# Kernel optimization log

Measured on AMD Instinct MI355X. Metric: run time of the kernel, lower is better.

## Reference

```python
import jax, jax.numpy as jnp
import numpy as np

H, KV, D = 12, 4, 128  # n_head, n_kv_head, head_dim
VE_GATE_CH = 12

def _rmsnorm(x):
    eps = jnp.finfo(x.dtype).eps  # matches torch F.rms_norm default eps
    return x * jax.lax.rsqrt(jnp.mean(x * x, axis=-1, keepdims=True) + eps)

def _rope(x, cos, sin):
    d = x.shape[-1] // 2
    x1, x2 = x[..., :d], x[..., d:]
    return jnp.concatenate([x1 * cos + x2 * sin, -x1 * sin + x2 * cos], axis=-1)

def setup_inputs() -> dict:
    key = jax.random.key(0)
    ks = jax.random.split(key, 9)
    B, T, C = 2, 2048, 1536
    x = jax.random.normal(ks[0], (B, T, C), jnp.float32)
    ve = jax.random.normal(ks[1], (B, T, KV * D), jnp.float32)
    ang = jax.random.uniform(ks[2], (1, T, 1, D // 2), jnp.float32) * (2.0 * np.pi)
    cos, sin = jnp.cos(ang), jnp.sin(ang)
    Wq = jax.random.normal(ks[3], (H * D, C), jnp.float32) * 0.02
    Wk = jax.random.normal(ks[4], (KV * D, C), jnp.float32) * 0.02
    Wv = jax.random.normal(ks[5], (KV * D, C), jnp.float32) * 0.02
    Wproj = jax.random.normal(ks[6], (C, C), jnp.float32) * 0.02
    Wg = jax.random.normal(ks[7], (KV, VE_GATE_CH), jnp.float32) * 0.02
    return dict(x=x, ve=ve, cos=cos, sin=sin, Wq=Wq, Wk=Wk, Wv=Wv, Wproj=Wproj, Wg=Wg, window=1024)

def reference(x, ve, cos, sin, Wq, Wk, Wv, Wproj, Wg, window):
    B, T, C = x.shape
    q = (x @ Wq.T).reshape(B, T, H, D)
    k = (x @ Wk.T).reshape(B, T, KV, D)
    v = (x @ Wv.T).reshape(B, T, KV, D)
    # value-embedding gate: 3*sigmoid(Linear(x[..., :12])) per kv head
    gate = 3.0 * jax.nn.sigmoid(x[..., :VE_GATE_CH] @ Wg.T)  # [B,T,KV]
    v = v + gate[..., None] * ve.reshape(B, T, KV, D)
    q = _rmsnorm(_rope(q, cos, sin)) * 1.2
    k = _rmsnorm(_rope(k, cos, sin)) * 1.2
    rep = H // KV  # GQA group size
    qh = q.transpose(0, 2, 1, 3).reshape(B, KV, rep, T, D)
    kh = k.transpose(0, 2, 1, 3)  # [B,KV,T,D]
    vh = v.transpose(0, 2, 1, 3)
    scores = jnp.einsum('bgrtd,bgsd->bgrts', qh, kh) / np.sqrt(D)
    row = jnp.arange(T)[:, None]
    col = jnp.arange(T)[None, :]
    if window < 0 or window >= T:
        mask = col <= row  # pure causal
    else:
        mask = (col <= row) & (row - col <= window)  # causal sliding window
    scores = jnp.where(mask, scores, -jnp.inf)
    att = jax.nn.softmax(scores, axis=-1)
    y = jnp.einsum('bgrts,bgsd->bgrtd', att, vh)
    y = y.reshape(B, H, T, D).transpose(0, 2, 1, 3).reshape(B, T, H * D)
    return y @ Wproj.T
```

## Files before the change

kernel.cpp:

```cpp
#include <hip/hip_runtime.h>
#include <hip/hip_bf16.h>
#include <math.h>

#define B_  2
#define T_  2048
#define C_  1536
#define H_  12
#define KV_ 4
#define D_  128
#define M_  (B_*T_)
#define REP_ (H_/KV_)
#define NQKV_ 2560
#define KK_  1536
#define NKT_ 24

typedef __bf16 bf16x8 __attribute__((ext_vector_type(8)));
typedef float  f32x4  __attribute__((ext_vector_type(4)));
typedef unsigned u32x4 __attribute__((ext_vector_type(4)));

union BCast { u32x4 u; bf16x8 b; };

__device__ inline bf16x8 ldb8(const ushort* p) {
    BCast c; c.u = *reinterpret_cast<const u32x4*>(p); return c.b;
}

__device__ inline ushort f2bf(float f) {
    union { float f; unsigned u; } v; v.f = f;
    unsigned u = v.u;
    return (ushort)((u + 0x7FFF + ((u >> 16) & 1)) >> 16);
}

__device__ inline float bf2f(ushort u) {
    union { unsigned u; float f; } v; v.u = (unsigned)u << 16;
    return v.f;
}

__device__ inline void async_copy16(const ushort* g, ushort* l) {
    __builtin_amdgcn_global_load_lds(
        (const __attribute__((address_space(1))) unsigned*)g,
        (__attribute__((address_space(3))) unsigned*)l, 16, 0, 0);
}

__device__ __host__ inline int dperm(int d) {
    return (d < 32) ? d : (d < 64 ? d + 32 : (d < 96 ? d - 32 : d));
}

#define MFMA16(va, vb, d) d = __builtin_amdgcn_mfma_f32_16x16x32_bf16(va, vb, d, 0, 0, 0)

template<int EPI>
__global__ __launch_bounds__(256, 2) void gemm128(const ushort* __restrict__ A,
                                                  const ushort* __restrict__ Bm,
                                                  ushort* __restrict__ Qp,
                                                  ushort* __restrict__ Kp,
                                                  ushort* __restrict__ Vt,
                                                  float* __restrict__ Cf,
                                                  const float* __restrict__ cosb,
                                                  const float* __restrict__ sinb,
                                                  const float* __restrict__ xf,
                                                  const float* __restrict__ ve,
                                                  const float* __restrict__ Wg) {
    __shared__ ushort smem[32768];
    ushort* ldsA = smem;
    ushort* ldsB = smem + 16384;
    const int tid  = threadIdx.x;
    const int wave = tid >> 6, lane = tid & 63;
    const int m16 = lane & 15, quad = lane >> 4;
    const int WM = wave >> 1, WN = wave & 1;

    const int nwg  = gridDim.x * gridDim.y;
    const int orig = blockIdx.y * gridDim.x + blockIdx.x;
    const int vid  = (orig & 7) * (nwg >> 3) + (orig >> 3);
    const int bxT  = vid >> 5;
    const int byT  = vid & 31;
    const int bm = byT << 7, bn = bxT << 7;

    const int r = tid >> 3;
    const int slot8 = ((tid & 7) ^ (r & 7)) << 3;
    const ushort* Ag = A  + (size_t)(bm + r) * KK_ + slot8;
    const ushort* Bg = Bm + (size_t)(bn + r) * KK_ + slot8;
    const size_t row32 = (size_t)32 * KK_;

    auto stage = [&](const ushort* Gp, ushort* ldsOp, int kc) {
        ushort* base = ldsOp + wave * 512;
        const ushort* g = Gp + kc;
        async_copy16(g,             base);
        async_copy16(g +   row32,   base + 2048);
        async_copy16(g + 2*row32,   base + 4096);
        async_copy16(g + 3*row32,   base + 6144);
    };

    const int swzu = (m16 & 7) << 3;
    const int k0u  = (quad * 8) ^ swzu;
    const int k1u  = (32 + quad * 8) ^ swzu;
    const ushort* aB0 = ldsA + ((WM * 64 + m16) << 6) + k0u;
    const ushort* aB1 = ldsA + ((WM * 64 + m16) << 6) + k1u;
    const ushort* bB0 = ldsB + ((WN * 64 + m16) << 6) + k0u;
    const ushort* bB1 = ldsB + ((WN * 64 + m16) << 6) + k1u;

    f32x4 acc[4][4];
    #pragma unroll
    for (int i = 0; i < 4; i++)
        #pragma unroll
        for (int j = 0; j < 4; j++) acc[i][j] = (f32x4){0.f, 0.f, 0.f, 0.f};

    stage(Bg, ldsB, 0);         stage(Ag, ldsA, 0);
    stage(Bg, ldsB + 8192, 64); stage(Ag, ldsA + 8192, 64);
    __builtin_amdgcn_s_waitcnt(0x0F78);
    __builtin_amdgcn_sched_barrier(0);
    __builtin_amdgcn_s_barrier();
    __builtin_amdgcn_sched_barrier(0);

    #pragma unroll 1
    for (int kt = 0; kt < NKT_; kt++) {
        const int bo = (kt & 1) ? 8192 : 0;
        bf16x8 a[8], b[8];
        #pragma unroll
        for (int mf = 0; mf < 4; mf++) {
            a[mf*2+0] = ldb8(aB0 + bo + mf*1024);
            a[mf*2+1] = ldb8(aB1 + bo + mf*1024);
        }
        #pragma unroll
        for (int nf = 0; nf < 4; nf++) {
            b[nf*2+0] = ldb8(bB0 + bo + nf*1024);
            b[nf*2+1] = ldb8(bB1 + bo + nf*1024);
        }
        __builtin_amdgcn_s_setprio(1);
        #pragma unroll
        for (int mf = 0; mf < 4; mf++)
            #pragma unroll
            for (int nf = 0; nf < 4; nf++) {
                MFMA16(a[mf*2+0], b[nf*2+0], acc[mf][nf]);
                MFMA16(a[mf*2+1], b[nf*2+1], acc[mf][nf]);
            }
        __builtin_amdgcn_s_setprio(0);
        if (kt < NKT_ - 1) {
            __builtin_amdgcn_sched_barrier(0);
            __builtin_amdgcn_s_barrier();
            __builtin_amdgcn_sched_barrier(0);
            if (kt < NKT_ - 2) {
                stage(Bg, ldsB + ((kt & 1) ? 8192 : 0), (kt + 2) << 6);
                stage(Ag, ldsA + ((kt & 1) ? 8192 : 0), (kt + 2) << 6);
                __builtin_amdgcn_s_waitcnt(0x0F78);
            } else {
                __builtin_amdgcn_s_waitcnt(0x0F70);
            }
            __builtin_amdgcn_sched_barrier(0);
            __builtin_amdgcn_s_barrier();
            __builtin_amdgcn_sched_barrier(0);
        }
    }
    __syncthreads();

    if constexpr (EPI == 0) {
        if (bn >= 2048) {
            const int g  = (bn - 2048) >> 7;
            const int bb = bm >> 11;
            const int tb = bm & (T_ - 1);
            ushort* tile = smem;
            float* gateS = (float*)(smem + 128 * 130);
            #pragma unroll
            for (int mf = 0; mf < 4; mf++)
                #pragma unroll
                for (int reg = 0; reg < 4; reg++) {
                    const int tl = WM*64 + mf*16 + quad*4 + reg;
                    #pragma unroll
                    for (int nf = 0; nf < 4; nf++) {
                        const int d = WN*64 + nf*16 + m16;
                        tile[d*130 + tl] = f2bf(acc[mf][nf][reg]);
                    }
                }
            if (tid < 128) {
                const float* xr = xf + (size_t)(bb * T_ + tb + tid) * C_;
                float a = 0.f;
                #pragma unroll
                for (int c = 0; c < 12; c++) a += xr[c] * Wg[g * 12 + c];
                gateS[tid] = 3.0f / (1.0f + __expf(-a));
            }
            __syncthreads();
            const float* veb = ve + (size_t)(bb * T_ + tb) * 512 + g * D_;
            #pragma unroll
            for (int i = 0; i < 64; i++) {
                const int idx = i * 256 + tid;
                const int tl = idx >> 7, d = idx & 127;
                const float vv = bf2f(tile[d*130 + tl])
                               + gateS[tl] * veb[(size_t)tl * 512 + d];
                tile[d*130 + tl] = f2bf(vv);
            }
            __syncthreads();
            ushort* ob = Vt + ((size_t)(bb * KV_ + g) * D_) * T_ + tb;
            #pragma unroll
            for (int i = 0; i < 64; i++) {
                const int idx = i * 256 + tid;
                const int d = idx >> 7, c = idx & 127;
                ob[(size_t)d * T_ + c] = tile[d*130 + c];
            }
        } else {
            float* ssqS = (float*)ldsA;
            #pragma unroll
            for (int mf = 0; mf < 4; mf++) {
                #pragma unroll
                for (int reg = 0; reg < 4; reg++) {
                    float v = acc[mf][0][reg]*acc[mf][0][reg] + acc[mf][1][reg]*acc[mf][1][reg]
                            + acc[mf][2][reg]*acc[mf][2][reg] + acc[mf][3][reg]*acc[mf][3][reg];
                    v += __shfl_xor(v, 1); v += __shfl_xor(v, 2);
                    v += __shfl_xor(v, 4); v += __shfl_xor(v, 8);
                    if (m16 == 0) {
                        const int rl = WM*64 + mf*16 + quad*4 + reg;
                        ssqS[rl*2 + WN] = v;
                    }
                }
            }
            __syncthreads();

            const bool isq = (bn < 1536);
            const float osc = isq ? (1.2f * 1.2f * 0.08838834764831845f) : 1.0f;
            const int hh  = isq ? (bn >> 7) : ((bn - 1536) >> 7);
            const int nh  = isq ? H_ : KV_;
            ushort* outp  = isq ? Qp : Kp;

            #pragma unroll
            for (int mf = 0; mf < 4; mf++) {
                #pragma unroll
                for (int reg = 0; reg < 4; reg++) {
                    const int rl = WM*64 + mf*16 + quad*4 + reg;
                    const int row = bm + rl;
                    const float tot = ssqS[rl*2] + ssqS[rl*2 + 1];
                    const float sc = rsqrtf(tot * (1.0f/128.0f) + 1.1920928955078125e-07f) * osc;
                    const int b = row >> 11, t = row & (T_ - 1);
                    ushort* orow = outp + ((size_t)(b * nh + hh) * T_ + t) * D_;
                    #pragma unroll
                    for (int nf = 0; nf < 2; nf++) {
                        const int ipair = WN * 32 + nf*16 + m16;
                        const float c = cosb[t*64 + ipair], s = sinb[t*64 + ipair];
                        const float x1 = acc[mf][nf][reg], x2 = acc[mf][nf+2][reg];
                        const int oc = WN * 64 + nf*16 + m16;
                        orow[oc]      = f2bf((x1*c + x2*s) * sc);
                        orow[oc + 32] = f2bf((x2*c - x1*s) * sc);
                    }
                }
            }
        }
    } else {
        #pragma unroll
        for (int mf = 0; mf < 4; mf++) {
            const int rl = WM*64 + mf*16 + quad*4;
            #pragma unroll
            for (int reg = 0; reg < 4; reg++) {
                float* cr = Cf + (size_t)(bm + rl + reg) * C_ + bn + WN*64 + m16;
                #pragma unroll
                for (int nf = 0; nf < 4; nf++)
                    cr[nf*16] = acc[mf][nf][reg];
            }
        }
    }
}

#define SEG0 1572864
#define SEG1 2162688
#define SEG2 2359296
#define SEG3 2555904
#define SEG4 3145728
#define ROW4 384
__global__ __launch_bounds__(256) void cast_all(const float* __restrict__ x,
                                                const float* __restrict__ Wq,
                                                const float* __restrict__ Wk,
                                                const float* __restrict__ Wv,
                                                const float* __restrict__ Wp,
                                                ushort* __restrict__ xb,
                                                ushort* __restrict__ Wqkvb,
                                                ushort* __restrict__ Wpb) {
    const int i = blockIdx.x * 256 + threadIdx.x;
    float4 v; size_t dst4; ushort* dstp;
    if (i < SEG0) {
        v = ((const float4*)x)[i]; dstp = xb; dst4 = i;
    } else if (i < SEG1) {
        const int j = i - SEG0;
        const int r = j / ROW4, c4 = j - r * ROW4;
        const int d = r & 127, hh = r >> 7;
        v = ((const float4*)Wq)[j]; dstp = Wqkvb;
        dst4 = (size_t)(hh * 128 + dperm(d)) * ROW4 + c4;
    } else if (i < SEG2) {
        const int j = i - SEG1;
        const int r = j / ROW4, c4 = j - r * ROW4;
        const int d = r & 127, g = r >> 7;
        v = ((const float4*)Wk)[j]; dstp = Wqkvb;
        dst4 = (size_t)(1536 + g * 128 + dperm(d)) * ROW4 + c4;
    } else if (i < SEG3) {
        const int j = i - SEG2;
        v = ((const float4*)Wv)[j]; dstp = Wqkvb;
        dst4 = (size_t)2048 * ROW4 + j;
    } else {
        const int j = i - SEG3;
        v = ((const float4*)Wp)[j]; dstp = Wpb; dst4 = j;
    }
    ((ushort4*)dstp)[dst4] = make_ushort4(f2bf(v.x), f2bf(v.y), f2bf(v.z), f2bf(v.w));
}

__global__ __launch_bounds__(256, 3) void attn_mfma(const ushort* __restrict__ Qp,
                                                    const ushort* __restrict__ Kp,
                                                    const ushort* __restrict__ Vt,
                                                    ushort* __restrict__ Y,
                                                    const int* __restrict__ wptr) {
    const int t0 = blockIdx.x * 64;
    const int h  = blockIdx.y, b = blockIdx.z;
    const int g  = h / REP_;
    const int tid  = threadIdx.x;
    const int wave = tid >> 6, lane = tid & 63;
    const int m16 = lane & 15, quad = lane >> 4;

    __shared__ ushort Ks[2][4096];
    __shared__ ushort Vs[2][4096];
    __shared__ ushort Pl[4][16 * 40];

    const int w = *wptr;
    const bool windowed = (w >= 0 && w < T_);
    const unsigned wu = windowed ? (unsigned)w : 0x7FFFFFFFu;
    int s_lo = 0;
    if (windowed) { s_lo = t0 - w; if (s_lo < 0) s_lo = 0; }
    const int s_hi = t0 + 63;
    const int ss0 = s_lo & ~31;
    const int NST = ((s_hi - ss0) >> 5) + 1;
    const int tw = t0 + wave * 16;

    const ushort* qrow = Qp + ((size_t)(b * H_ + h) * T_ + tw + m16) * D_ + quad * 8;
    bf16x8 qa[4];
    #pragma unroll
    for (int kc = 0; kc < 4; kc++) qa[kc] = ldb8(qrow + kc * 32);

    const ushort* kbase = Kp + (size_t)(b * KV_ + g) * T_ * D_;
    const ushort* vbase = Vt + (size_t)(b * KV_ + g) * D_ * T_;

    const int c0 = wave, c1 = wave + 4;
    const ushort* kg0 = kbase + (size_t)((c0 & 1) * 16 + (lane >> 2)) * D_ + (c0 >> 1) * 32 + (lane & 3) * 8;
    const ushort* kg1 = kbase + (size_t)((c1 & 1) * 16 + (lane >> 2)) * D_ + (c1 >> 1) * 32 + (lane & 3) * 8;
    const ushort* vg0 = vbase + (size_t)(c0 * 16 + (lane >> 2)) * T_ + (lane & 3) * 8;
    const ushort* vg1 = vbase + (size_t)(c1 * 16 + (lane >> 2)) * T_ + (lane & 3) * 8;
    const int kl0o = c0 * 512, kl1o = c1 * 512;

    auto stg = [&](int st, int buf) {
        const int ss = ss0 + (st << 5);
        const size_t koff = (size_t)ss * D_;
        async_copy16(kg0 + koff, Ks[buf] + kl0o);
        async_copy16(kg1 + koff, Ks[buf] + kl1o);
        async_copy16(vg0 + ss,   Vs[buf] + kl0o);
        async_copy16(vg1 + ss,   Vs[buf] + kl1o);
    };

    f32x4 o[8];
    #pragma unroll
    for (int dt = 0; dt < 8; dt++) o[dt] = (f32x4){0.f, 0.f, 0.f, 0.f};
    f32x4 lacc = (f32x4){0.f, 0.f, 0.f, 0.f};
    BCast onesc; onesc.u = (u32x4){0x3F803F80u, 0x3F803F80u, 0x3F803F80u, 0x3F803F80u};
    const bf16x8 ones = onesc.b;
    ushort* pw = &Pl[wave][0];

    stg(0, 0); stg(1, 1);
    __builtin_amdgcn_s_waitcnt(0x0F74);
    __builtin_amdgcn_sched_barrier(0);
    __builtin_amdgcn_s_barrier();
    __builtin_amdgcn_sched_barrier(0);

    #pragma unroll 1
    for (int st = 0; st < NST; st++) {
        const int ss = ss0 + (st << 5);
        const ushort* KsB = Ks[st & 1];
        const ushort* VsB = Vs[st & 1];

        f32x4 s0 = (f32x4){0.f,0.f,0.f,0.f};
        f32x4 s1 = (f32x4){0.f,0.f,0.f,0.f};
        #pragma unroll
        for (int kc = 0; kc < 4; kc++) {
            bf16x8 kf0 = ldb8(KsB + kc * 1024 + m16 * 32 + quad * 8);
            bf16x8 kf1 = ldb8(KsB + kc * 1024 + (16 + m16) * 32 + quad * 8);
            s0 = __builtin_amdgcn_mfma_f32_16x16x32_bf16(qa[kc], kf0, s0, 0, 0, 0);
            s1 = __builtin_amdgcn_mfma_f32_16x16x32_bf16(qa[kc], kf1, s1, 0, 0, 0);
        }

        const int sA = ss + m16, sB = ss + 16 + m16;
        #pragma unroll
        for (int reg = 0; reg < 4; reg++) {
            const int t = tw + quad * 4 + reg;
            const float pa = ((unsigned)(t - sA) <= wu) ? __expf(s0[reg]) : 0.f;
            const float pb = ((unsigned)(t - sB) <= wu) ? __expf(s1[reg]) : 0.f;
            pw[(quad * 4 + reg) * 40 + m16]      = f2bf(pa);
            pw[(quad * 4 + reg) * 40 + 16 + m16] = f2bf(pb);
        }

        __builtin_amdgcn_s_waitcnt(0xc07f);
        bf16x8 pfrag = ldb8(pw + m16 * 40 + quad * 8);

        #pragma unroll
        for (int dt = 0; dt < 8; dt++) {
            bf16x8 vf = ldb8(VsB + (dt * 16 + m16) * 32 + quad * 8);
            o[dt] = __builtin_amdgcn_mfma_f32_16x16x32_bf16(pfrag, vf, o[dt], 0, 0, 0);
        }
        lacc = __builtin_amdgcn_mfma_f32_16x16x32_bf16(pfrag, ones, lacc, 0, 0, 0);

        if (st < NST - 1) {
            __builtin_amdgcn_sched_barrier(0);
            __builtin_amdgcn_s_barrier();
            __builtin_amdgcn_sched_barrier(0);
            if (st < NST - 2) {
                stg(st + 2, st & 1);
                __builtin_amdgcn_s_waitcnt(0x0F74);
            } else {
                __builtin_amdgcn_s_waitcnt(0x0F70);
            }
            __builtin_amdgcn_sched_barrier(0);
            __builtin_amdgcn_s_barrier();
            __builtin_amdgcn_sched_barrier(0);
        }
    }

    float inv[4];
    #pragma unroll
    for (int reg = 0; reg < 4; reg++) inv[reg] = 1.0f / lacc[reg];
    ushort* yb = Y + ((size_t)(b * T_ + tw + quad * 4) * H_ + h) * D_ + m16;
    #pragma unroll
    for (int reg = 0; reg < 4; reg++)
        #pragma unroll
        for (int dt = 0; dt < 8; dt++)
            yb[(size_t)reg * H_ * D_ + dt * 16] = f2bf(o[dt][reg] * inv[reg]);
}

extern "C" void kernel_launch(void* const* d_in, const int* in_sizes, int n_in,
                              void* d_out, int out_size, void* d_ws, size_t ws_size,
                              hipStream_t stream) {
    const float* x     = (const float*)d_in[0];
    const float* ve    = (const float*)d_in[1];
    const float* cosb  = (const float*)d_in[2];
    const float* sinb  = (const float*)d_in[3];
    const float* Wq    = (const float*)d_in[4];
    const float* Wk    = (const float*)d_in[5];
    const float* Wv    = (const float*)d_in[6];
    const float* Wproj = (const float*)d_in[7];
    const float* Wg    = (const float*)d_in[8];
    const int*   wptr  = (const int*)d_in[9];
    float* out = (float*)d_out;

    ushort* xb    = (ushort*)d_ws;
    ushort* vbuf  = xb    + (size_t)M_ * C_;
    ushort* Qp    = vbuf  + (size_t)M_ * 512;
    ushort* Kp    = Qp    + (size_t)M_ * C_;
    ushort* Vt    = Kp    + (size_t)M_ * 512;
    ushort* yb16  = Vt    + (size_t)M_ * 512;
    ushort* Wqkvb = yb16  + (size_t)M_ * C_;
    ushort* Wpb   = Wqkvb + (size_t)NQKV_ * C_;

    cast_all<<<SEG4 / 256, 256, 0, stream>>>(x, Wq, Wk, Wv, Wproj, xb, Wqkvb, Wpb);

    gemm128<0><<<dim3(NQKV_ / 128, M_ / 128), 256, 0, stream>>>(
        xb, Wqkvb, Qp, Kp, Vt, nullptr, cosb, sinb, x, ve, Wg);

    attn_mfma<<<dim3(T_ / 64, H_, B_), 256, 0, stream>>>(Qp, Kp, Vt, yb16, wptr);

    gemm128<1><<<dim3(C_ / 128, M_ / 128), 256, 0, stream>>>(
        yb16, Wpb, nullptr, nullptr, nullptr, out, nullptr, nullptr,
        nullptr, nullptr, nullptr);
}
```

Measured before the change: 238.5 us.

## Load K/V fragments directly from global memory in attention, dropping LDS staging

The attention kernel no longer stages K and V tiles into double-buffered shared memory with async copies and block barriers. Each wave now loads its MFMA K and V fragments straight from global memory (relying on L2/L1 for reuse across the four waves), and the occupancy hint in launch_bounds is removed. This is meant to remove barrier synchronisation and LDS traffic. The cost is redundant global loads per wave and no explicit prefetch to hide memory latency.

Result: slower. 372.3 us (+56.1%).

```diff
diff --git a/kernel.cpp b/kernel.cpp
--- a/kernel.cpp
+++ b/kernel.cpp
@@ -296,11 +296,11 @@
     ((ushort4*)dstp)[dst4] = make_ushort4(f2bf(v.x), f2bf(v.y), f2bf(v.z), f2bf(v.w));
 }
 
-__global__ __launch_bounds__(256, 3) void attn_mfma(const ushort* __restrict__ Qp,
-                                                    const ushort* __restrict__ Kp,
-                                                    const ushort* __restrict__ Vt,
-                                                    ushort* __restrict__ Y,
-                                                    const int* __restrict__ wptr) {
+__global__ __launch_bounds__(256) void attn_mfma(const ushort* __restrict__ Qp,
+                                                 const ushort* __restrict__ Kp,
+                                                 const ushort* __restrict__ Vt,
+                                                 ushort* __restrict__ Y,
+                                                 const int* __restrict__ wptr) {
     const int t0 = blockIdx.x * 64;
     const int h  = blockIdx.y, b = blockIdx.z;
     const int g  = h / REP_;
@@ -308,8 +308,6 @@
     const int wave = tid >> 6, lane = tid & 63;
     const int m16 = lane & 15, quad = lane >> 4;
 
-    __shared__ ushort Ks[2][4096];
-    __shared__ ushort Vs[2][4096];
     __shared__ ushort Pl[4][16 * 40];
 
     const int w = *wptr;
@@ -319,7 +317,6 @@
     if (windowed) { s_lo = t0 - w; if (s_lo < 0) s_lo = 0; }
     const int s_hi = t0 + 63;
     const int ss0 = s_lo & ~31;
-    const int NST = ((s_hi - ss0) >> 5) + 1;
     const int tw = t0 + wave * 16;
 
     const ushort* qrow = Qp + ((size_t)(b * H_ + h) * T_ + tw + m16) * D_ + quad * 8;
@@ -327,24 +324,8 @@
     #pragma unroll
     for (int kc = 0; kc < 4; kc++) qa[kc] = ldb8(qrow + kc * 32);
 
-    const ushort* kbase = Kp + (size_t)(b * KV_ + g) * T_ * D_;
-    const ushort* vbase = Vt + (size_t)(b * KV_ + g) * D_ * T_;
-
-    const int c0 = wave, c1 = wave + 4;
-    const ushort* kg0 = kbase + (size_t)((c0 & 1) * 16 + (lane >> 2)) * D_ + (c0 >> 1) * 32 + (lane & 3) * 8;
-    const ushort* kg1 = kbase + (size_t)((c1 & 1) * 16 + (lane >> 2)) * D_ + (c1 >> 1) * 32 + (lane & 3) * 8;
-    const ushort* vg0 = vbase + (size_t)(c0 * 16 + (lane >> 2)) * T_ + (lane & 3) * 8;
-    const ushort* vg1 = vbase + (size_t)(c1 * 16 + (lane >> 2)) * T_ + (lane & 3) * 8;
-    const int kl0o = c0 * 512, kl1o = c1 * 512;
-
-    auto stg = [&](int st, int buf) {
-        const int ss = ss0 + (st << 5);
-        const size_t koff = (size_t)ss * D_;
-        async_copy16(kg0 + koff, Ks[buf] + kl0o);
-        async_copy16(kg1 + koff, Ks[buf] + kl1o);
-        async_copy16(vg0 + ss,   Vs[buf] + kl0o);
-        async_copy16(vg1 + ss,   Vs[buf] + kl1o);
-    };
+    const ushort* kfb = Kp + (size_t)(b * KV_ + g) * T_ * D_ + (size_t)m16 * D_ + quad * 8;
+    const ushort* vfb = Vt + (size_t)(b * KV_ + g) * D_ * T_ + (size_t)m16 * T_ + quad * 8;
 
     f32x4 o[8];
     #pragma unroll
@@ -354,24 +335,15 @@
     const bf16x8 ones = onesc.b;
     ushort* pw = &Pl[wave][0];
 
-    stg(0, 0); stg(1, 1);
-    __builtin_amdgcn_s_waitcnt(0x0F74);
-    __builtin_amdgcn_sched_barrier(0);
-    __builtin_amdgcn_s_barrier();
-    __builtin_amdgcn_sched_barrier(0);
-
     #pragma unroll 1
-    for (int st = 0; st < NST; st++) {
-        const int ss = ss0 + (st << 5);
-        const ushort* KsB = Ks[st & 1];
-        const ushort* VsB = Vs[st & 1];
-
+    for (int ss = ss0; ss <= s_hi; ss += 32) {
+        const ushort* kr0 = kfb + (size_t)ss * D_;
         f32x4 s0 = (f32x4){0.f,0.f,0.f,0.f};
         f32x4 s1 = (f32x4){0.f,0.f,0.f,0.f};
         #pragma unroll
         for (int kc = 0; kc < 4; kc++) {
-            bf16x8 kf0 = ldb8(KsB + kc * 1024 + m16 * 32 + quad * 8);
-            bf16x8 kf1 = ldb8(KsB + kc * 1024 + (16 + m16) * 32 + quad * 8);
+            bf16x8 kf0 = ldb8(kr0 + kc * 32);
+            bf16x8 kf1 = ldb8(kr0 + 16 * D_ + kc * 32);
             s0 = __builtin_amdgcn_mfma_f32_16x16x32_bf16(qa[kc], kf0, s0, 0, 0, 0);
             s1 = __builtin_amdgcn_mfma_f32_16x16x32_bf16(qa[kc], kf1, s1, 0, 0, 0);
         }
@@ -391,25 +363,10 @@
 
         #pragma unroll
         for (int dt = 0; dt < 8; dt++) {
-            bf16x8 vf = ldb8(VsB + (dt * 16 + m16) * 32 + quad * 8);
+            bf16x8 vf = ldb8(vfb + (size_t)(dt * 16) * T_ + ss);
             o[dt] = __builtin_amdgcn_mfma_f32_16x16x32_bf16(pfrag, vf, o[dt], 0, 0, 0);
         }
         lacc = __builtin_amdgcn_mfma_f32_16x16x32_bf16(pfrag, ones, lacc, 0, 0, 0);
-
-        if (st < NST - 1) {
-            __builtin_amdgcn_sched_barrier(0);
-            __builtin_amdgcn_s_barrier();
-            __builtin_amdgcn_sched_barrier(0);
-            if (st < NST - 2) {
-                stg(st + 2, st & 1);
-                __builtin_amdgcn_s_waitcnt(0x0F74);
-            } else {
-                __builtin_amdgcn_s_waitcnt(0x0F70);
-            }
-            __builtin_amdgcn_sched_barrier(0);
-            __builtin_amdgcn_s_barrier();
-            __builtin_amdgcn_sched_barrier(0);
-        }
     }
 
     float inv[4];
```

## Process two 64-row query tiles per attention block to reuse K/V tiles

Applied to the files above, without the earlier changes.

Each attention workgroup now handles 128 query rows instead of 64. Each wave computes two 16-row query sub-tiles against the same shared K/V stages, so the K/V global loads and LDS staging are amortized over twice the work. The cost is doubled accumulator registers, dropping the occupancy hint of 3, and half as many blocks (384), which hurts load balance and latency hiding. Causal/window tiles are now coarser, so the lower half computes some extra fully masked stages.

Result: slower. 256.3 us (+7.5%).

```diff
diff --git a/kernel.cpp b/kernel.cpp
--- a/kernel.cpp
+++ b/kernel.cpp
@@ -296,12 +296,12 @@
     ((ushort4*)dstp)[dst4] = make_ushort4(f2bf(v.x), f2bf(v.y), f2bf(v.z), f2bf(v.w));
 }
 
-__global__ __launch_bounds__(256, 3) void attn_mfma(const ushort* __restrict__ Qp,
-                                                    const ushort* __restrict__ Kp,
-                                                    const ushort* __restrict__ Vt,
-                                                    ushort* __restrict__ Y,
-                                                    const int* __restrict__ wptr) {
-    const int t0 = blockIdx.x * 64;
+__global__ __launch_bounds__(256) void attn_mfma(const ushort* __restrict__ Qp,
+                                                 const ushort* __restrict__ Kp,
+                                                 const ushort* __restrict__ Vt,
+                                                 ushort* __restrict__ Y,
+                                                 const int* __restrict__ wptr) {
+    const int t0 = blockIdx.x * 128;
     const int h  = blockIdx.y, b = blockIdx.z;
     const int g  = h / REP_;
     const int tid  = threadIdx.x;
@@ -310,22 +310,26 @@
 
     __shared__ ushort Ks[2][4096];
     __shared__ ushort Vs[2][4096];
-    __shared__ ushort Pl[4][16 * 40];
+    __shared__ ushort Pl[4][2][16 * 40];
 
     const int w = *wptr;
     const bool windowed = (w >= 0 && w < T_);
     const unsigned wu = windowed ? (unsigned)w : 0x7FFFFFFFu;
     int s_lo = 0;
     if (windowed) { s_lo = t0 - w; if (s_lo < 0) s_lo = 0; }
-    const int s_hi = t0 + 63;
+    const int s_hi = t0 + 127;
     const int ss0 = s_lo & ~31;
     const int NST = ((s_hi - ss0) >> 5) + 1;
-    const int tw = t0 + wave * 16;
-
-    const ushort* qrow = Qp + ((size_t)(b * H_ + h) * T_ + tw + m16) * D_ + quad * 8;
-    bf16x8 qa[4];
+    const int twA = t0 + wave * 16;
+    const int twB = t0 + 64 + wave * 16;
+
+    const ushort* qbase = Qp + (size_t)(b * H_ + h) * T_ * D_;
+    bf16x8 qaA[4], qaB[4];
     #pragma unroll
-    for (int kc = 0; kc < 4; kc++) qa[kc] = ldb8(qrow + kc * 32);
+    for (int kc = 0; kc < 4; kc++) {
+        qaA[kc] = ldb8(qbase + (size_t)(twA + m16) * D_ + kc * 32 + quad * 8);
+        qaB[kc] = ldb8(qbase + (size_t)(twB + m16) * D_ + kc * 32 + quad * 8);
+    }
 
     const ushort* kbase = Kp + (size_t)(b * KV_ + g) * T_ * D_;
     const ushort* vbase = Vt + (size_t)(b * KV_ + g) * D_ * T_;
@@ -346,13 +350,18 @@
         async_copy16(vg1 + ss,   Vs[buf] + kl1o);
     };
 
-    f32x4 o[8];
+    f32x4 oA[8], oB[8];
     #pragma unroll
-    for (int dt = 0; dt < 8; dt++) o[dt] = (f32x4){0.f, 0.f, 0.f, 0.f};
-    f32x4 lacc = (f32x4){0.f, 0.f, 0.f, 0.f};
+    for (int dt = 0; dt < 8; dt++) {
+        oA[dt] = (f32x4){0.f, 0.f, 0.f, 0.f};
+        oB[dt] = (f32x4){0.f, 0.f, 0.f, 0.f};
+    }
+    f32x4 laccA = (f32x4){0.f, 0.f, 0.f, 0.f};
+    f32x4 laccB = (f32x4){0.f, 0.f, 0.f, 0.f};
     BCast onesc; onesc.u = (u32x4){0x3F803F80u, 0x3F803F80u, 0x3F803F80u, 0x3F803F80u};
     const bf16x8 ones = onesc.b;
-    ushort* pw = &Pl[wave][0];
+    ushort* pwA = &Pl[wave][0][0];
+    ushort* pwB = &Pl[wave][1][0];
 
     stg(0, 0); stg(1, 1);
     __builtin_amdgcn_s_waitcnt(0x0F74);
@@ -366,35 +375,47 @@
         const ushort* KsB = Ks[st & 1];
         const ushort* VsB = Vs[st & 1];
 
-        f32x4 s0 = (f32x4){0.f,0.f,0.f,0.f};
-        f32x4 s1 = (f32x4){0.f,0.f,0.f,0.f};
+        f32x4 s0A = (f32x4){0.f,0.f,0.f,0.f};
+        f32x4 s1A = (f32x4){0.f,0.f,0.f,0.f};
+        f32x4 s0B = (f32x4){0.f,0.f,0.f,0.f};
+        f32x4 s1B = (f32x4){0.f,0.f,0.f,0.f};
         #pragma unroll
         for (int kc = 0; kc < 4; kc++) {
             bf16x8 kf0 = ldb8(KsB + kc * 1024 + m16 * 32 + quad * 8);
             bf16x8 kf1 = ldb8(KsB + kc * 1024 + (16 + m16) * 32 + quad * 8);
-            s0 = __builtin_amdgcn_mfma_f32_16x16x32_bf16(qa[kc], kf0, s0, 0, 0, 0);
-            s1 = __builtin_amdgcn_mfma_f32_16x16x32_bf16(qa[kc], kf1, s1, 0, 0, 0);
+            s0A = __builtin_amdgcn_mfma_f32_16x16x32_bf16(qaA[kc], kf0, s0A, 0, 0, 0);
+            s1A = __builtin_amdgcn_mfma_f32_16x16x32_bf16(qaA[kc], kf1, s1A, 0, 0, 0);
+            s0B = __builtin_amdgcn_mfma_f32_16x16x32_bf16(qaB[kc], kf0, s0B, 0, 0, 0);
+            s1B = __builtin_amdgcn_mfma_f32_16x16x32_bf16(qaB[kc], kf1, s1B, 0, 0, 0);
         }
 
         const int sA = ss + m16, sB = ss + 16 + m16;
         #pragma unroll
         for (int reg = 0; reg < 4; reg++) {
-            const int t = tw + quad * 4 + reg;
-            const float pa = ((unsigned)(t - sA) <= wu) ? __expf(s0[reg]) : 0.f;
-            const float pb = ((unsigned)(t - sB) <= wu) ? __expf(s1[reg]) : 0.f;
-            pw[(quad * 4 + reg) * 40 + m16]      = f2bf(pa);
-            pw[(quad * 4 + reg) * 40 + 16 + m16] = f2bf(pb);
+            const int tA = twA + quad * 4 + reg;
+            const int tB = twB + quad * 4 + reg;
+            const float paA = ((unsigned)(tA - sA) <= wu) ? __expf(s0A[reg]) : 0.f;
+            const float pbA = ((unsigned)(tA - sB) <= wu) ? __expf(s1A[reg]) : 0.f;
+            const float paB = ((unsigned)(tB - sA) <= wu) ? __expf(s0B[reg]) : 0.f;
+            const float pbB = ((unsigned)(tB - sB) <= wu) ? __expf(s1B[reg]) : 0.f;
+            pwA[(quad * 4 + reg) * 40 + m16]      = f2bf(paA);
+            pwA[(quad * 4 + reg) * 40 + 16 + m16] = f2bf(pbA);
+            pwB[(quad * 4 + reg) * 40 + m16]      = f2bf(paB);
+            pwB[(quad * 4 + reg) * 40 + 16 + m16] = f2bf(pbB);
         }
 
         __builtin_amdgcn_s_waitcnt(0xc07f);
-        bf16x8 pfrag = ldb8(pw + m16 * 40 + quad * 8);
+        bf16x8 pfA = ldb8(pwA + m16 * 40 + quad * 8);
+        bf16x8 pfB = ldb8(pwB + m16 * 40 + quad * 8);
 
         #pragma unroll
         for (int dt = 0; dt < 8; dt++) {
             bf16x8 vf = ldb8(VsB + (dt * 16 + m16) * 32 + quad * 8);
-            o[dt] = __builtin_amdgcn_mfma_f32_16x16x32_bf16(pfrag, vf, o[dt], 0, 0, 0);
-        }
-        lacc = __builtin_amdgcn_mfma_f32_16x16x32_bf16(pfrag, ones, lacc, 0, 0, 0);
+            oA[dt] = __builtin_amdgcn_mfma_f32_16x16x32_bf16(pfA, vf, oA[dt], 0, 0, 0);
+            oB[dt] = __builtin_amdgcn_mfma_f32_16x16x32_bf16(pfB, vf, oB[dt], 0, 0, 0);
+        }
+        laccA = __builtin_amdgcn_mfma_f32_16x16x32_bf16(pfA, ones, laccA, 0, 0, 0);
+        laccB = __builtin_amdgcn_mfma_f32_16x16x32_bf16(pfB, ones, laccB, 0, 0, 0);
 
         if (st < NST - 1) {
             __builtin_amdgcn_sched_barrier(0);
@@ -412,15 +433,21 @@
         }
     }
 
-    float inv[4];
+    float invA[4], invB[4];
     #pragma unroll
-    for (int reg = 0; reg < 4; reg++) inv[reg] = 1.0f / lacc[reg];
-    ushort* yb = Y + ((size_t)(b * T_ + tw + quad * 4) * H_ + h) * D_ + m16;
+    for (int reg = 0; reg < 4; reg++) {
+        invA[reg] = 1.0f / laccA[reg];
+        invB[reg] = 1.0f / laccB[reg];
+    }
+    ushort* ybA = Y + ((size_t)(b * T_ + twA + quad * 4) * H_ + h) * D_ + m16;
+    ushort* ybB = Y + ((size_t)(b * T_ + twB + quad * 4) * H_ + h) * D_ + m16;
     #pragma unroll
     for (int reg = 0; reg < 4; reg++)
         #pragma unroll
-        for (int dt = 0; dt < 8; dt++)
-            yb[(size_t)reg * H_ * D_ + dt * 16] = f2bf(o[dt][reg] * inv[reg]);
+        for (int dt = 0; dt < 8; dt++) {
+            ybA[(size_t)reg * H_ * D_ + dt * 16] = f2bf(oA[dt][reg] * invA[reg]);
+            ybB[(size_t)reg * H_ * D_ + dt * 16] = f2bf(oB[dt][reg] * invB[reg]);
+        }
 }
 
 extern "C" void kernel_launch(void* const* d_in, const int* in_sizes, int n_in,
@@ -452,7 +479,7 @@
     gemm128<0><<<dim3(NQKV_ / 128, M_ / 128), 256, 0, stream>>>(
         xb, Wqkvb, Qp, Kp, Vt, nullptr, cosb, sinb, x, ve, Wg);
 
-    attn_mfma<<<dim3(T_ / 64, H_, B_), 256, 0, stream>>>(Qp, Kp, Vt, yb16, wptr);
+    attn_mfma<<<dim3(T_ / 128, H_, B_), 256, 0, stream>>>(Qp, Kp, Vt, yb16, wptr);
 
     gemm128<1><<<dim3(C_ / 128, M_ / 128), 256, 0, stream>>>(
         yb16, Wpb, nullptr, nullptr, nullptr, out, nullptr, nullptr,
```
